# Optimization experiments

Hardware: AMD Instinct MI355X
Metric: run time of the kernel (lower is better)

## Reference

```python
import jax, jax.numpy as jnp
import numpy as np

NUM_NODES, FEAT_DIM, DIM, CLIPS = 100000, 128, 128, 8
S1, S2 = 10, 10
B, L = 1024, 8


def setup_inputs() -> dict:
    key = jax.random.key(0)
    k1, k2, k3, k4, k5 = jax.random.split(key, 5)
    features = jax.random.normal(k1, (NUM_NODES, FEAT_DIM), dtype=jnp.float32)
    # xavier-uniform-ish init for the per-clip projection
    local_weight = jax.random.normal(k2, (CLIPS, DIM, FEAT_DIM), dtype=jnp.float32) * (2.0 / (DIM + FEAT_DIM)) ** 0.5
    nodes = jax.random.randint(k3, (B, L), 0, NUM_NODES, dtype=jnp.int64 if jax.config.jax_enable_x64 else jnp.int32)
    neigh1 = jax.random.randint(k4, (NUM_NODES, S1), 0, NUM_NODES, dtype=nodes.dtype)
    neigh2 = jax.random.randint(k5, (NUM_NODES, S2), 0, NUM_NODES, dtype=nodes.dtype)
    return {"features": features, "local_weight": local_weight, "nodes": nodes,
            "neigh1": neigh1, "neigh2": neigh2}


def reference(features, local_weight, nodes, neigh1, neigh2):
    b, l = nodes.shape
    nf = nodes.reshape(-1)                     # [N] flat nodes
    # hop-0: raw features
    feat_self = features[nf]                   # [N, d]
    # hop-1: mean over sampled 1-hop neighbors (agg1)
    feats1 = features[neigh1[nf]].mean(axis=1)  # [N, s1, d] -> [N, d]
    # hop-2: mean over sampled 2-hop neighbors of agg1 outputs (agg2)
    two_hop = neigh1[neigh2[nf]]               # [N, s2, s1]
    feats2 = features[two_hop].mean(axis=2).mean(axis=1)  # [N, d]
    # per-clip projection: einsum('ckd,dn->ckn').permute(2,0,1) == 'ckd,nd->nck'
    outs = [jnp.einsum('ckd,nd->nck', local_weight, f)
            for f in (feats1, feats2, feat_self)]         # each [N, clips, dim]
    local = jnp.concatenate(outs, axis=-1)                # [N, clips, 3*dim]
    local = local.reshape(b, l, local_weight.shape[0], -1)
    return jax.nn.relu(local)
```

## Files before the change

kernel.cpp:

```cpp
#include <hip/hip_runtime.h>

typedef __attribute__((ext_vector_type(8))) short bf16x8;
typedef __attribute__((ext_vector_type(4))) float f32x4;

static constexpr int N_NODES = 8192;
static constexpr int FEAT    = 128;
static constexpr int NB      = 16;
static constexpr int NBLK    = N_NODES / NB;
static constexpr int XS      = 136;
static constexpr int FEAT_BLOCKS = 6250;

__device__ __forceinline__ unsigned short f2bf(float f) {
    unsigned u = __builtin_bit_cast(unsigned, f);
    u += 0x7FFFu + ((u >> 16) & 1u);
    return (unsigned short)(u >> 16);
}
__device__ __forceinline__ float bf2f(unsigned short h) {
    return __builtin_bit_cast(float, ((unsigned)h) << 16);
}
__device__ __forceinline__ unsigned f2fp8(float f) {
    unsigned u = __builtin_bit_cast(unsigned, f);
    unsigned s = (u >> 24) & 0x80u;
    float af = __builtin_bit_cast(float, u & 0x7fffffffu);
    if (!(af < 448.f)) af = 448.f;
    unsigned q = __builtin_bit_cast(unsigned, af * 0x1p-120f);
    unsigned b = (q + 0x7FFFFu + ((q >> 20) & 1u)) >> 20;
    return s | b;
}
__device__ __forceinline__ void acc8(float* a, const uint4 v) {
    a[0] += bf2f((unsigned short)(v.x & 0xffffu));
    a[1] += bf2f((unsigned short)(v.x >> 16));
    a[2] += bf2f((unsigned short)(v.y & 0xffffu));
    a[3] += bf2f((unsigned short)(v.y >> 16));
    a[4] += bf2f((unsigned short)(v.z & 0xffffu));
    a[5] += bf2f((unsigned short)(v.z >> 16));
    a[6] += bf2f((unsigned short)(v.w & 0xffffu));
    a[7] += bf2f((unsigned short)(v.w >> 16));
}
__device__ __forceinline__ void acc8f8(float* a, const uint2 v) {
#pragma unroll
    for (int i = 0; i < 4; ++i) {
        unsigned t = v.x << (24 - 8 * i);
        unsigned w = (unsigned)((int)t >> 4) & 0x87F00000u;
        a[i] = fmaf(__builtin_bit_cast(float, w), 0x1p120f, a[i]);
    }
#pragma unroll
    for (int i = 0; i < 4; ++i) {
        unsigned t = v.y << (24 - 8 * i);
        unsigned w = (unsigned)((int)t >> 4) & 0x87F00000u;
        a[4 + i] = fmaf(__builtin_bit_cast(float, w), 0x1p120f, a[4 + i]);
    }
}
__device__ __forceinline__ uint4 pack8(const float* a, float sc) {
    uint4 o;
    o.x = (unsigned)f2bf(a[0] * sc) | ((unsigned)f2bf(a[1] * sc) << 16);
    o.y = (unsigned)f2bf(a[2] * sc) | ((unsigned)f2bf(a[3] * sc) << 16);
    o.z = (unsigned)f2bf(a[4] * sc) | ((unsigned)f2bf(a[5] * sc) << 16);
    o.w = (unsigned)f2bf(a[6] * sc) | ((unsigned)f2bf(a[7] * sc) << 16);
    return o;
}

__global__ void __launch_bounds__(256) pack_all(
    const float* __restrict__ feat, const float* __restrict__ lw,
    unsigned short* __restrict__ T, unsigned char* __restrict__ T8,
    unsigned short* __restrict__ Wp)
{
    const int b = blockIdx.x;
    if (b < FEAT_BLOCKS) {
        const size_t i = (size_t)b * 256 + threadIdx.x;
        const f32x4* src = (const f32x4*)feat;
        const f32x4 v0 = __builtin_nontemporal_load(src + i * 2);
        const f32x4 v1 = __builtin_nontemporal_load(src + i * 2 + 1);
        ushort4 o0, o1;
        o0.x = f2bf(v0[0]); o0.y = f2bf(v0[1]); o0.z = f2bf(v0[2]); o0.w = f2bf(v0[3]);
        o1.x = f2bf(v1[0]); o1.y = f2bf(v1[1]); o1.z = f2bf(v1[2]); o1.w = f2bf(v1[3]);
        ((ushort4*)T)[i * 2]     = o0;
        ((ushort4*)T)[i * 2 + 1] = o1;
        uint2 p;
        p.x = f2fp8(v0[0]) | (f2fp8(v0[1]) << 8) | (f2fp8(v0[2]) << 16) | (f2fp8(v0[3]) << 24);
        p.y = f2fp8(v1[0]) | (f2fp8(v1[1]) << 8) | (f2fp8(v1[2]) << 16) | (f2fp8(v1[3]) << 24);
        ((uint2*)T8)[i] = p;
    } else {
        const int i = (b - FEAT_BLOCKS) * 256 + threadIdx.x;
        const float4 v = ((const float4*)lw)[i];
        ushort4 o;
        o.x = f2bf(v.x); o.y = f2bf(v.y); o.z = f2bf(v.z); o.w = f2bf(v.w);
        ((ushort4*)Wp)[i] = o;
    }
}

__global__ void __launch_bounds__(256) fused_enc(
    const unsigned short* __restrict__ T,
    const unsigned char*  __restrict__ T8,
    const int*   __restrict__ nodes,
    const int*   __restrict__ n1,
    const int*   __restrict__ n2,
    const unsigned short* __restrict__ Wp,
    float* __restrict__ out)
{
    __shared__ int nfs[NB];
    __shared__ int sm_m[NB][10];
    __shared__ int idx[NB][112];
    __shared__ unsigned short X[3 * NB][XS];

    const int blk = blockIdx.x;
    const int tid = threadIdx.x;

    if (tid < NB) nfs[tid] = nodes[blk * NB + tid];
    __syncthreads();
    if (tid < NB * 10) {
        const int i = tid / 10, s = tid - (tid / 10) * 10;
        idx[i][s] = n1[nfs[i] * 10 + s];
    }
    if (tid >= 96) {
        const int t = tid - 96;
        const int i = t / 10, s = t - (t / 10) * 10;
        sm_m[i][s] = n2[nfs[i] * 10 + s];
    }
    if (tid < NB) idx[tid][110] = nfs[tid];
    __syncthreads();
    for (int t = tid; t < NB * 100; t += 256) {
        const int i = t / 100, rr = t - (t / 100) * 100;
        idx[i][10 + rr] = n1[sm_m[i][rr / 10] * 10 + (rr - (rr / 10) * 10)];
    }
    __syncthreads();

    {
        const int g = tid >> 4;
        const int l = tid & 15;
        const unsigned short* Tl  = T  + l * 8;
        const unsigned char*  Tl8 = T8 + l * 8;

        float aA[8] = {0,0,0,0,0,0,0,0};
        float aB[8] = {0,0,0,0,0,0,0,0};

        {
            uint4 v[10];
#pragma unroll
            for (int s = 0; s < 10; ++s)
                v[s] = *(const uint4*)(Tl + (size_t)idx[g][s] * FEAT);
#pragma unroll
            for (int s = 0; s < 10; ++s) acc8(aA, v[s]);
        }
#pragma unroll
        for (int c = 1; c <= 10; ++c) {
            uint2 v8[10];
#pragma unroll
            for (int s = 0; s < 10; ++s)
                v8[s] = *(const uint2*)(Tl8 + (size_t)idx[g][c * 10 + s] * FEAT);
#pragma unroll
            for (int s = 0; s < 10; ++s) acc8f8(aB, v8[s]);
        }
        const uint4 sv = *(const uint4*)(Tl + (size_t)idx[g][110] * FEAT);
        *(uint4*)&X[g * 3 + 2][l * 8] = sv;
        *(uint4*)&X[g * 3 + 0][l * 8] = pack8(aA, 0.1f);
        *(uint4*)&X[g * 3 + 1][l * 8] = pack8(aB, 0.01f);
    }
    __syncthreads();

    const int wave = tid >> 6;
    const int lane = tid & 63;
    const int r = lane & 15;
    const int q = lane >> 4;

#pragma unroll
    for (int ch = 0; ch < 4; ++ch) {
        const int yBase = wave * 256 + ch * 64;
        f32x4 acc[3][4];
#pragma unroll
        for (int mt = 0; mt < 3; ++mt)
#pragma unroll
            for (int nj = 0; nj < 4; ++nj) acc[mt][nj] = (f32x4){0.f, 0.f, 0.f, 0.f};

#pragma unroll
        for (int k0 = 0; k0 < 4; ++k0) {
            bf16x8 a[3], b[4];
#pragma unroll
            for (int mt = 0; mt < 3; ++mt)
                a[mt] = *(const bf16x8*)&X[mt * 16 + r][k0 * 32 + q * 8];
#pragma unroll
            for (int nj = 0; nj < 4; ++nj)
                b[nj] = *(const bf16x8*)(Wp + (size_t)(yBase + nj * 16 + r) * FEAT
                                            + q * 8 + k0 * 32);
#pragma unroll
            for (int mt = 0; mt < 3; ++mt)
#pragma unroll
                for (int nj = 0; nj < 4; ++nj)
                    acc[mt][nj] = __builtin_amdgcn_mfma_f32_16x16x32_bf16(
                        a[mt], b[nj], acc[mt][nj], 0, 0, 0);
        }

#pragma unroll
        for (int mt = 0; mt < 3; ++mt) {
#pragma unroll
            for (int i = 0; i < 4; ++i) {
                const int xl = mt * 16 + q * 4 + i;
                const int nl = xl / 3;
                const int j  = xl - nl * 3;
                float* orow = out + (size_t)(blk * NB + nl) * 3072 + j * 128;
#pragma unroll
                for (int nj = 0; nj < 4; ++nj) {
                    const int y = yBase + nj * 16 + r;
                    const int c = y >> 7;
                    const int k = y & 127;
                    orow[c * 384 + k] = fmaxf(acc[mt][nj][i], 0.f);
                }
            }
        }
    }
}

extern "C" void kernel_launch(void* const* d_in, const int* in_sizes, int n_in,
                              void* d_out, int out_size, void* d_ws, size_t ws_size,
                              hipStream_t stream) {
    const float* features = (const float*)d_in[0];
    const float* lw       = (const float*)d_in[1];
    const int*   nodes    = (const int*)d_in[2];
    const int*   n1       = (const int*)d_in[3];
    const int*   n2       = (const int*)d_in[4];
    float*       out      = (float*)d_out;

    unsigned short* Wp = (unsigned short*)d_ws;
    unsigned short* T  = Wp + (size_t)1024 * FEAT;
    unsigned char*  T8 = (unsigned char*)(T + (size_t)100000 * FEAT);

    pack_all<<<FEAT_BLOCKS + 128, 256, 0, stream>>>(features, lw, T, T8, Wp);
    fused_enc<<<NBLK, 256, 0, stream>>>(T, T8, nodes, n1, n2, Wp, out);
}
```

Before: 61.37 us.

## Drop bf16 feature table; gather hop-1 from fp8 and self from fp32

Removes the bf16 copy of the full feature table so the pack kernel only writes the fp8 table, processing 16 elements per thread. Hop-1 neighbor features are now gathered from fp8 instead of bf16, and self features are read directly from the fp32 input. The gather loop is software-pipelined across clip groups. This cuts pack-kernel write traffic at the cost of lower precision for the hop-1 mean.

```diff
diff --git a/kernel.cpp b/kernel.cpp
--- a/kernel.cpp
+++ b/kernel.cpp
@@ -8,15 +8,12 @@
 static constexpr int NB      = 16;
 static constexpr int NBLK    = N_NODES / NB;
 static constexpr int XS      = 136;
-static constexpr int FEAT_BLOCKS = 6250;
+static constexpr int F8_BLOCKS = 3125;
 
 __device__ __forceinline__ unsigned short f2bf(float f) {
     unsigned u = __builtin_bit_cast(unsigned, f);
     u += 0x7FFFu + ((u >> 16) & 1u);
     return (unsigned short)(u >> 16);
-}
-__device__ __forceinline__ float bf2f(unsigned short h) {
-    return __builtin_bit_cast(float, ((unsigned)h) << 16);
 }
 __device__ __forceinline__ unsigned f2fp8(float f) {
     unsigned u = __builtin_bit_cast(unsigned, f);
@@ -27,16 +24,6 @@
     unsigned b = (q + 0x7FFFFu + ((q >> 20) & 1u)) >> 20;
     return s | b;
 }
-__device__ __forceinline__ void acc8(float* a, const uint4 v) {
-    a[0] += bf2f((unsigned short)(v.x & 0xffffu));
-    a[1] += bf2f((unsigned short)(v.x >> 16));
-    a[2] += bf2f((unsigned short)(v.y & 0xffffu));
-    a[3] += bf2f((unsigned short)(v.y >> 16));
-    a[4] += bf2f((unsigned short)(v.z & 0xffffu));
-    a[5] += bf2f((unsigned short)(v.z >> 16));
-    a[6] += bf2f((unsigned short)(v.w & 0xffffu));
-    a[7] += bf2f((unsigned short)(v.w >> 16));
-}
 __device__ __forceinline__ void acc8f8(float* a, const uint2 v) {
 #pragma unroll
     for (int i = 0; i < 4; ++i) {
@@ -62,26 +49,22 @@
 
 __global__ void __launch_bounds__(256) pack_all(
     const float* __restrict__ feat, const float* __restrict__ lw,
-    unsigned short* __restrict__ T, unsigned char* __restrict__ T8,
-    unsigned short* __restrict__ Wp)
+    unsigned char* __restrict__ T8, unsigned short* __restrict__ Wp)
 {
     const int b = blockIdx.x;
-    if (b < FEAT_BLOCKS) {
+    if (b < F8_BLOCKS) {
         const size_t i = (size_t)b * 256 + threadIdx.x;
-        const f32x4* src = (const f32x4*)feat;
-        const f32x4 v0 = __builtin_nontemporal_load(src + i * 2);
-        const f32x4 v1 = __builtin_nontemporal_load(src + i * 2 + 1);
-        ushort4 o0, o1;
-        o0.x = f2bf(v0[0]); o0.y = f2bf(v0[1]); o0.z = f2bf(v0[2]); o0.w = f2bf(v0[3]);
-        o1.x = f2bf(v1[0]); o1.y = f2bf(v1[1]); o1.z = f2bf(v1[2]); o1.w = f2bf(v1[3]);
-        ((ushort4*)T)[i * 2]     = o0;
-        ((ushort4*)T)[i * 2 + 1] = o1;
-        uint2 p;
-        p.x = f2fp8(v0[0]) | (f2fp8(v0[1]) << 8) | (f2fp8(v0[2]) << 16) | (f2fp8(v0[3]) << 24);
-        p.y = f2fp8(v1[0]) | (f2fp8(v1[1]) << 8) | (f2fp8(v1[2]) << 16) | (f2fp8(v1[3]) << 24);
-        ((uint2*)T8)[i] = p;
+        const f32x4* src = (const f32x4*)feat + i * 4;
+        uint4 p;
+        unsigned* pw = (unsigned*)&p;
+#pragma unroll
+        for (int h = 0; h < 4; ++h) {
+            const f32x4 v = __builtin_nontemporal_load(src + h);
+            pw[h] = f2fp8(v[0]) | (f2fp8(v[1]) << 8) | (f2fp8(v[2]) << 16) | (f2fp8(v[3]) << 24);
+        }
+        ((uint4*)T8)[i] = p;
     } else {
-        const int i = (b - FEAT_BLOCKS) * 256 + threadIdx.x;
+        const int i = (b - F8_BLOCKS) * 256 + threadIdx.x;
         const float4 v = ((const float4*)lw)[i];
         ushort4 o;
         o.x = f2bf(v.x); o.y = f2bf(v.y); o.z = f2bf(v.z); o.w = f2bf(v.w);
@@ -90,8 +73,8 @@
 }
 
 __global__ void __launch_bounds__(256) fused_enc(
-    const unsigned short* __restrict__ T,
     const unsigned char*  __restrict__ T8,
+    const float* __restrict__ featF,
     const int*   __restrict__ nodes,
     const int*   __restrict__ n1,
     const int*   __restrict__ n2,
@@ -128,31 +111,40 @@
     {
         const int g = tid >> 4;
         const int l = tid & 15;
-        const unsigned short* Tl  = T  + l * 8;
-        const unsigned char*  Tl8 = T8 + l * 8;
+        const unsigned char* Tl8 = T8 + l * 8;
 
         float aA[8] = {0,0,0,0,0,0,0,0};
         float aB[8] = {0,0,0,0,0,0,0,0};
-
-        {
-            uint4 v[10];
+        uint2 va[10], vb[10];
+
+#pragma unroll
+        for (int s = 0; s < 10; ++s)
+            va[s] = *(const uint2*)(Tl8 + (size_t)idx[g][s] * FEAT);
+        const float* Fs = featF + (size_t)idx[g][110] * FEAT + l * 8;
+        const f32x4 s0 = *(const f32x4*)Fs;
+        const f32x4 s1 = *(const f32x4*)(Fs + 4);
+
+#pragma unroll
+        for (int cc = 0; cc < 5; ++cc) {
+            const int cA = 2 * cc + 1, cB = 2 * cc + 2;
 #pragma unroll
             for (int s = 0; s < 10; ++s)
-                v[s] = *(const uint4*)(Tl + (size_t)idx[g][s] * FEAT);
-#pragma unroll
-            for (int s = 0; s < 10; ++s) acc8(aA, v[s]);
-        }
-#pragma unroll
-        for (int c = 1; c <= 10; ++c) {
-            uint2 v8[10];
+                vb[s] = *(const uint2*)(Tl8 + (size_t)idx[g][cA * 10 + s] * FEAT);
+#pragma unroll
+            for (int s = 0; s < 10; ++s) {
+                if (cc == 0) acc8f8(aA, va[s]); else acc8f8(aB, va[s]);
+            }
 #pragma unroll
             for (int s = 0; s < 10; ++s)
-                v8[s] = *(const uint2*)(Tl8 + (size_t)idx[g][c * 10 + s] * FEAT);
-#pragma unroll
-            for (int s = 0; s < 10; ++s) acc8f8(aB, v8[s]);
-        }
-        const uint4 sv = *(const uint4*)(Tl + (size_t)idx[g][110] * FEAT);
-        *(uint4*)&X[g * 3 + 2][l * 8] = sv;
+                va[s] = *(const uint2*)(Tl8 + (size_t)idx[g][cB * 10 + s] * FEAT);
+#pragma unroll
+            for (int s = 0; s < 10; ++s) acc8f8(aB, vb[s]);
+        }
+#pragma unroll
+        for (int s = 0; s < 10; ++s) acc8f8(aB, va[s]);
+
+        float aS[8] = {s0[0], s0[1], s0[2], s0[3], s1[0], s1[1], s1[2], s1[3]};
+        *(uint4*)&X[g * 3 + 2][l * 8] = pack8(aS, 1.0f);
         *(uint4*)&X[g * 3 + 0][l * 8] = pack8(aA, 0.1f);
         *(uint4*)&X[g * 3 + 1][l * 8] = pack8(aB, 0.01f);
     }
@@ -221,9 +213,8 @@
     float*       out      = (float*)d_out;
 
     unsigned short* Wp = (unsigned short*)d_ws;
-    unsigned short* T  = Wp + (size_t)1024 * FEAT;
-    unsigned char*  T8 = (unsigned char*)(T + (size_t)100000 * FEAT);
-
-    pack_all<<<FEAT_BLOCKS + 128, 256, 0, stream>>>(features, lw, T, T8, Wp);
-    fused_enc<<<NBLK, 256, 0, stream>>>(T, T8, nodes, n1, n2, Wp, out);
-}
+    unsigned char*  T8 = (unsigned char*)(Wp + (size_t)1024 * FEAT);
+
+    pack_all<<<F8_BLOCKS + 128, 256, 0, stream>>>(features, lw, T8, Wp);
+    fused_enc<<<NBLK, 256, 0, stream>>>(T8, features, nodes, n1, n2, Wp, out);
+}
```

Result: slower. 81.68 us (+33.1%).
